# Optimization experiments

Hardware: AMD Instinct MI355X
Metric: run time of the kernel (lower is better)

Reference implementation:

```python
import jax, jax.numpy as jnp
import numpy as np

NUM_HEADS = 8
NUM_KV_HEADS = 2
PATCH = 16
STRIDE = 8
HORIZON = 96
NQ = 3
EPS_RMS = 1e-6
EPS_REVIN = 1e-5


def rms_norm(x, scale):
    return x * jax.lax.rsqrt(jnp.mean(x * x, axis=-1, keepdims=True) + EPS_RMS) * scale


def lstm_scan(xs, wi, wh, b):
    # xs: (N, T, Din); flax OptimizedLSTMCell gate order i, f, g, o
    N = xs.shape[0]
    H = wh.shape[0]

    def step(carry, x_t):
        c, h = carry
        z = x_t @ wi + h @ wh + b
        i, f, g, o = jnp.split(z, 4, axis=-1)
        c = jax.nn.sigmoid(f) * c + jax.nn.sigmoid(i) * jnp.tanh(g)
        h = jax.nn.sigmoid(o) * jnp.tanh(c)
        return (c, h), h

    init = (jnp.zeros((N, H), xs.dtype), jnp.zeros((N, H), xs.dtype))
    _, hs = jax.lax.scan(step, init, jnp.swapaxes(xs, 0, 1))
    return jnp.swapaxes(hs, 0, 1)  # (N, T, H)


def gqa(x, wq, wk, wv, wo):
    # x: (B, S, D); non-causal grouped-query attention
    B, S, D = x.shape
    hd = wq.shape[1] // NUM_HEADS
    q = (x @ wq).reshape(B, S, NUM_HEADS, hd)
    k = (x @ wk).reshape(B, S, NUM_KV_HEADS, hd)
    v = (x @ wv).reshape(B, S, NUM_KV_HEADS, hd)
    rep = NUM_HEADS // NUM_KV_HEADS
    k = jnp.repeat(k, rep, axis=2)
    v = jnp.repeat(v, rep, axis=2)
    scale = jnp.asarray(1.0 / np.sqrt(hd), x.dtype)
    attn = jax.nn.softmax(jnp.einsum('bqhd,bkhd->bhqk', q, k) * scale, axis=-1)
    out = jnp.einsum('bhqk,bkhd->bqhd', attn, v).reshape(B, S, NUM_HEADS * hd)
    return out @ wo, attn


def setup_inputs() -> dict:
    key = jax.random.key(0)
    ks = jax.random.split(key, 12)
    b, d, m, T = 8, 16, 8, 512
    H, H2 = 256, 512
    NB = 4

    def w(k, shape, fan_in):
        return jax.random.normal(k, shape, jnp.float32) / np.sqrt(fan_in)

    return {
        'series': jax.random.normal(ks[0], (b, d, m, T), jnp.float32),
        'revin_scale': jnp.ones((m,), jnp.float32),
        'revin_bias': jnp.zeros((m,), jnp.float32),
        'up_w': w(ks[1], (PATCH, H), PATCH),
        'lstm_wi': w(ks[2], (NB, H, 4 * H2), H),
        'lstm_wh': w(ks[3], (NB, H2, 4 * H2), H2),
        'lstm_b': jnp.zeros((NB, 4 * H2), jnp.float32),
        'norm_scale': jnp.ones((NB, H2), jnp.float32),
        'wq': w(ks[4], (NB, H2, H2), H2),
        'wk': w(ks[5], (NB, H2, H2 // 4), H2),
        'wv': w(ks[6], (NB, H2, H2 // 4), H2),
        'wo': w(ks[7], (NB, H2, H2), H2),
        'down_w': w(ks[8], (NB, H2, H), H2),
        'head_norm_scale': jnp.ones((H,), jnp.float32),
        'point_w': w(ks[9], (H, HORIZON), H),
        'quant_w': w(ks[10], (H, HORIZON * NQ), H),
    }


def reference(series, revin_scale, revin_bias, up_w, lstm_wi, lstm_wh, lstm_b,
              norm_scale, wq, wk, wv, wo, down_w, head_norm_scale, point_w, quant_w):
    b, d, m, T = series.shape
    num_blocks = lstm_wi.shape[0]
    H = up_w.shape[1]
    H2 = lstm_wh.shape[1]

    # RevIN instance norm over time with per-metric affine
    mean = series.mean(axis=-1, keepdims=True)
    std = jnp.sqrt(series.var(axis=-1, keepdims=True) + EPS_REVIN)
    sc = revin_scale[:, None]
    bi = revin_bias[:, None]
    normed = (series - mean) / std * sc + bi

    # Patcher (seq_len=512, patch=16, stride=8 -> 63 patches, no padding needed)
    n_p = (T - PATCH) // STRIDE + 1
    idx = jnp.arange(n_p)[:, None] * STRIDE + jnp.arange(PATCH)
    patches = normed[..., idx]            # (b, d, m, np, ps)
    x = patches @ up_w                    # (b, d, m, np, H)

    for blk in range(num_blocks):
        s = x.reshape(b * d * m, n_p, H)
        hs = lstm_scan(s, lstm_wi[blk], lstm_wh[blk], lstm_b[blk])  # (bdm, np, H2)
        # '(b d m) np h -> (b m np) d h'
        hs = hs.reshape(b, d, m, n_p, H2).transpose(0, 2, 3, 1, 4).reshape(b * m * n_p, d, H2)
        nrm = rms_norm(hs, norm_scale[blk])
        mix, _ = gqa(nrm, wq[blk], wk[blk], wv[blk], wo[blk])
        bel = mix @ down_w[blk]           # (bmnp, d, H)
        # '(b m np) d h -> b d m np h'
        x = bel.reshape(b, m, n_p, d, H).transpose(0, 3, 1, 2, 4)

    # pooling_mode == 'last' with device mixer: last block's belief at last patch
    last = x[:, :, :, -1, :]              # (b, d, m, H)
    nb = rms_norm(last, head_norm_scale)
    point = nb @ point_w                  # (b, d, m, horizon)
    quant = (nb @ quant_w).reshape(b, d, m, HORIZON, NQ).transpose(4, 0, 1, 2, 3)

    def denorm(y):
        return (y - bi) / sc * std + mean

    point_u = denorm(point)
    quant_u = denorm(quant)               # broadcasts over leading quantile axis
    return jnp.concatenate([point_u[None], quant_u], axis=0)  # (1+NQ, b, d, m, horizon)
```

## Files before the change

kernel.cpp:

```cpp
#include <hip/hip_runtime.h>
#include <hip/hip_bf16.h>

#define NP 63

typedef __attribute__((ext_vector_type(8))) short short8;
typedef __attribute__((ext_vector_type(4))) float f32x4;
typedef __attribute__((ext_vector_type(4))) int i32x4;
typedef unsigned char uchar;

__device__ __forceinline__ float sigf(float x){ return 1.0f/(1.0f+expf(-x)); }
__device__ __forceinline__ float u2f(ushort u){ __hip_bfloat16 h; *(ushort*)&h = u; return __bfloat162float(h); }
__device__ __forceinline__ ushort f2u(float f){ __hip_bfloat16 h = __float2bfloat16(f); return *(ushort*)&h; }

__global__ void __launch_bounds__(256) k_revin(const float* __restrict__ series,
    float* __restrict__ meanv, float* __restrict__ stdv, int* __restrict__ bar)
{
  int n = blockIdx.x, tid = threadIdx.x;
  if(n==0 && tid<64) bar[tid] = 0;
  __shared__ float s1[256], s2[256];
  const float* p = series + n*512;
  float a = 0.f, b = 0.f;
  for(int t=tid;t<512;t+=256){ float v=p[t]; a+=v; b+=v*v; }
  s1[tid]=a; s2[tid]=b; __syncthreads();
  for(int s=128;s>0;s>>=1){
    if(tid<s){ s1[tid]+=s1[tid+s]; s2[tid]+=s2[tid+s]; }
    __syncthreads();
  }
  if(tid==0){
    float mu = s1[0]*(1.f/512.f);
    float var = fmaxf(s2[0]*(1.f/512.f) - mu*mu, 0.f);
    meanv[n]=mu; stdv[n]=sqrtf(var+1e-5f);
  }
}

__global__ void __launch_bounds__(256) k_patch(const float* __restrict__ series,
    const float* __restrict__ rs, const float* __restrict__ rb,
    const float* __restrict__ up_w, const float* __restrict__ meanv,
    const float* __restrict__ stdv, ushort* __restrict__ x)
{
  int n = blockIdx.x, tid = threadIdx.x;
  int m = n & 7;
  __shared__ float sn[512];
  float mu = meanv[n], sd = stdv[n];
  float A = rs[m]/sd, C = rb[m] - mu*A;
  const float* p = series + n*512;
  for(int t=tid;t<512;t+=256) sn[t] = p[t]*A + C;
  __syncthreads();
  float w[16];
  #pragma unroll
  for(int i=0;i<16;i++) w[i] = up_w[i*256+tid];
  ushort* xo = x + n*(NP*256);
  for(int pi=0;pi<NP;pi++){
    float acc=0.f;
    #pragma unroll
    for(int i=0;i<16;i++) acc = fmaf(sn[pi*8+i], w[i], acc);
    xo[pi*256+tid] = f2u(acc);
  }
}

__global__ void __launch_bounds__(256) k_wod(const float* __restrict__ wo,
    const float* __restrict__ dw, float* __restrict__ wod)
{
  int i = blockIdx.x, blk = blockIdx.y, tid = threadIdx.x;
  __shared__ float row[512];
  const float* wr = wo + (blk*512 + i)*512;
  for(int k=tid;k<512;k+=256) row[k]=wr[k];
  __syncthreads();
  const float* d = dw + blk*512*256;
  float acc=0.f;
  for(int k=0;k<512;k++) acc = fmaf(row[k], d[k*256+tid], acc);
  wod[(blk*512+i)*256+tid]=acc;
}

__global__ void __launch_bounds__(256) k_tr_wodt(const float* __restrict__ wod, ushort* __restrict__ wodt)
{
  __shared__ float tile[32][33];
  int blk = blockIdx.z;
  int n0 = blockIdx.x*32, k0 = blockIdx.y*32;
  int tid = threadIdx.x;
  #pragma unroll
  for(int i=0;i<4;i++){
    int idx = tid + 256*i; int kl = idx>>5, nl = idx&31;
    tile[kl][nl] = wod[blk*512*256 + (k0+kl)*256 + n0+nl];
  }
  __syncthreads();
  #pragma unroll
  for(int i=0;i<4;i++){
    int idx = tid + 256*i; int nl = idx>>5, kl = idx&31;
    wodt[blk*256*512 + (n0+nl)*512 + k0+kl] = f2u(tile[kl][nl]);
  }
}

__global__ void __launch_bounds__(256) k_tr_lstmw(const float* __restrict__ wi,
    const float* __restrict__ wh, ushort* __restrict__ wt)
{
  __shared__ float tile[32][33];
  int blk = blockIdx.z;
  int n0 = blockIdx.x*32, k0 = blockIdx.y*32;
  int tid = threadIdx.x;
  #pragma unroll
  for(int i=0;i<4;i++){
    int idx = tid + 256*i; int kl = idx>>5, nl = idx&31;
    int k = k0+kl, n = n0+nl;
    float v = (k<256) ? wi[blk*256*2048 + k*2048 + n]
                      : wh[blk*512*2048 + (k-256)*2048 + n];
    tile[kl][nl] = v;
  }
  __syncthreads();
  #pragma unroll
  for(int i=0;i<4;i++){
    int idx = tid + 256*i; int nl = idx>>5, kl = idx&31;
    wt[blk*2048*768 + (n0+nl)*768 + k0+kl] = f2u(tile[kl][nl]);
  }
}

__global__ void __launch_bounds__(256) k_tr_qkvw(const float* __restrict__ wq,
    const float* __restrict__ wk, const float* __restrict__ wv,
    const float* __restrict__ ns, ushort* __restrict__ wqkvt)
{
  __shared__ float tile[32][33];
  int blk = blockIdx.z;
  int n0 = blockIdx.x*32, k0 = blockIdx.y*32;
  int tid = threadIdx.x;
  #pragma unroll
  for(int i=0;i<4;i++){
    int idx = tid + 256*i; int kl = idx>>5, nl = idx&31;
    int k = k0+kl, n = n0+nl;
    float v;
    if(n < 512)      v = wq[blk*512*512 + k*512 + n];
    else if(n < 640) v = wk[blk*512*128 + k*128 + (n-512)];
    else             v = wv[blk*512*128 + k*128 + (n-640)];
    tile[kl][nl] = v * ns[blk*512 + k];
  }
  __syncthreads();
  #pragma unroll
  for(int i=0;i<4;i++){
    int idx = tid + 256*i; int nl = idx>>5, kl = idx&31;
    wqkvt[blk*768*512 + (n0+nl)*512 + k0+kl] = f2u(tile[kl][nl]);
  }
}

__global__ void __launch_bounds__(256,1) k_lstm_scan(
    const ushort* __restrict__ x, ushort* __restrict__ hs,
    const ushort* __restrict__ wt, const float* __restrict__ bias,
    uchar* __restrict__ flags, int tagbase)
{
  __shared__ __align__(16) short Bwh[128*512];
  __shared__ __align__(16) ushort hstage[64*32];
  int fb = blockIdx.x;
  int g = (fb & 7) | ((fb >> 4) & 8);
  int y = (fb >> 3) & 15;
  int n0 = g*64, jj0 = y*32;
  int tid = threadIdx.x;
  int wv = tid>>6, lane = tid&63, quad = lane>>4, l16 = lane&15;
  int wrow = wv>>1, wcol = wv&1;

  for(int i=tid; i<8192; i+=256){
    int c = i>>6, kb = i&63;
    short8 v = *(const short8*)(wt + ((c>>5)*512 + jj0 + (c&31))*768 + 256 + kb*8);
    *(short8*)((char*)Bwh + c*1024 + ((kb*16) ^ ((c&7)<<4))) = v;
  }
  int jj = jj0 + wcol*16 + l16;
  short8 bwi[4][8];
  #pragma unroll
  for(int gg=0; gg<4; gg++){
    const ushort* wp = wt + (gg*512 + jj)*768 + quad*8;
    #pragma unroll
    for(int ck=0; ck<8; ck++) bwi[gg][ck] = *(const short8*)(wp + ck*32);
  }
  float bI=bias[jj], bF=bias[512+jj], bG=bias[1024+jj], bO=bias[1536+jj];
  float cs[2][4];
  #pragma unroll
  for(int a=0;a<2;a++){
    #pragma unroll
    for(int r=0;r<4;r++) cs[a][r]=0.f;
  }
  const ushort* xb0 = x  + (n0 + wrow*32 + l16)*(NP*256) + quad*8;
  const ushort* hb0 = hs + (n0 + wrow*32 + l16)*(NP*512) + quad*8;
  int xorb = (l16&7)<<4;
  uchar* myflag = flags + g*16 + y;
  const uchar* gflags = flags + g*16;
  __syncthreads();

  for(int t=0; t<NP; ++t){
    f32x4 acc[4][2];
    #pragma unroll
    for(int gg=0; gg<4; gg++){ acc[gg][0]=(f32x4){0.f,0.f,0.f,0.f}; acc[gg][1]=(f32x4){0.f,0.f,0.f,0.f}; }

    #pragma unroll
    for(int ck=0; ck<8; ck++){
      short8 a0 = *(const short8*)(xb0 + t*256 + ck*32);
      short8 a1 = *(const short8*)(xb0 + 16*(NP*256) + t*256 + ck*32);
      #pragma unroll
      for(int gg=0; gg<4; gg++){
        acc[gg][0] = __builtin_amdgcn_mfma_f32_16x16x32_bf16(a0, bwi[gg][ck], acc[gg][0], 0,0,0);
        acc[gg][1] = __builtin_amdgcn_mfma_f32_16x16x32_bf16(a1, bwi[gg][ck], acc[gg][1], 0,0,0);
      }
    }

    if(t > 0){
      if(tid==0){
        uint tag = (uint)(tagbase + t);
        while(1){
          i32x4 f;
          asm volatile("global_load_dwordx4 %0, %1, off sc0 sc1\n\ts_waitcnt vmcnt(0)"
                       : "=&v"(f) : "v"(gflags) : "memory");
          uint ok = 1u;
          #pragma unroll
          for(int q=0;q<4;q++){
            uint w = (uint)f[q];
            if(( w      &0xffu) < tag) ok=0;
            if(((w>>8 ) &0xffu) < tag) ok=0;
            if(((w>>16) &0xffu) < tag) ok=0;
            if( (w>>24)         < tag) ok=0;
          }
          if(ok) break;
          __builtin_amdgcn_s_sleep(1);
        }
      }
      __syncthreads();

      const ushort* hb = hb0 + (t-1)*512;
      #pragma unroll
      for(int ck=0; ck<16; ck++){
        short8 a0 = *(const short8*)(hb + ck*32);
        short8 a1 = *(const short8*)(hb + 16*(NP*512) + ck*32);
        #pragma unroll
        for(int gg=0; gg<4; gg++){
          int c = gg*32 + wcol*16 + l16;
          short8 bh = *(short8*)((char*)Bwh + c*1024 + ((ck*64 + quad*16) ^ xorb));
          acc[gg][0] = __builtin_amdgcn_mfma_f32_16x16x32_bf16(a0, bh, acc[gg][0], 0,0,0);
          acc[gg][1] = __builtin_amdgcn_mfma_f32_16x16x32_bf16(a1, bh, acc[gg][1], 0,0,0);
        }
      }
    }

    #pragma unroll
    for(int a=0;a<2;a++){
      #pragma unroll
      for(int r=0;r<4;r++){
        int rowl = wrow*32 + a*16 + quad*4 + r;
        float zi=acc[0][a][r]+bI, zf=acc[1][a][r]+bF, zg=acc[2][a][r]+bG, zo=acc[3][a][r]+bO;
        float c = sigf(zf)*cs[a][r] + sigf(zi)*tanhf(zg);
        cs[a][r] = c;
        float hv = sigf(zo)*tanhf(c);
        int coll = wcol*16 + l16;
        int off = rowl*64 + ((coll*2) ^ (((rowl>>2)&3)<<4));
        *(ushort*)((char*)hstage + off) = f2u(hv);
      }
    }
    __syncthreads();
    {
      int rowl = tid>>2, c0b = (tid&3)*16;
      int off = rowl*64 + (c0b ^ (((rowl>>2)&3)<<4));
      i32x4 vv = *(const i32x4*)((const char*)hstage + off);
      ushort* gp = hs + ((size_t)(n0+rowl)*NP + t)*512 + jj0 + (tid&3)*8;
      asm volatile("global_store_dwordx4 %0, %1, off sc0 sc1" :: "v"(gp), "v"(vv) : "memory");
    }
    __syncthreads();
    if(tid==0 && t < NP-1){
      uint v = (uint)(tagbase + t + 1);
      asm volatile("global_store_byte %0, %1, off sc0 sc1" :: "v"(myflag), "v"(v) : "memory");
    }
  }
}

__global__ void __launch_bounds__(256) k_qkv_m(
    const ushort* __restrict__ hs, const ushort* __restrict__ wqkvt,
    ushort* __restrict__ qkv)
{
  __shared__ short As[128*40];
  __shared__ short Bs[128*40];
  __shared__ float rvs[128];
  int tid = threadIdx.x;
  int r0 = blockIdx.x*128, c0 = blockIdx.y*128;
  int wv = tid>>6, lane = tid&63, quad = lane>>4, l16 = lane&15;
  int wrow = wv>>1, wcol = wv&1;
  int arow0 = tid>>2, akp = tid&3;
  const ushort* aptr[2];
  #pragma unroll
  for(int i=0;i<2;i++){
    int r = r0 + arow0 + i*64;
    int bq = r/8064; int rr = r - bq*8064;
    int m = rr/1008; int rem = rr - m*1008;
    int p = rem>>4; int d = rem&15;
    int n = (bq*16+d)*8+m;
    aptr[i] = hs + (n*NP+p)*512 + akp*8;
  }
  f32x4 acc[4][4];
  #pragma unroll
  for(int b=0;b<4;b++){
    #pragma unroll
    for(int a=0;a<4;a++) acc[b][a] = (f32x4){0.f,0.f,0.f,0.f};
  }
  float ssq0 = 0.f, ssq1 = 0.f;
  for(int k0=0;k0<512;k0+=32){
    {
      short8 av = *(const short8*)(aptr[0] + k0);
      *(short8*)&As[arow0*40 + akp*8] = av;
      #pragma unroll
      for(int e=0;e<8;e++){ float vv = u2f((ushort)av[e]); ssq0 = fmaf(vv, vv, ssq0); }
    }
    {
      short8 av = *(const short8*)(aptr[1] + k0);
      *(short8*)&As[(arow0+64)*40 + akp*8] = av;
      #pragma unroll
      for(int e=0;e<8;e++){ float vv = u2f((ushort)av[e]); ssq1 = fmaf(vv, vv, ssq1); }
    }
    #pragma unroll
    for(int i=0;i<2;i++){
      int pc = tid + 256*i; int rl=pc>>2, kp=pc&3;
      *(short8*)&Bs[rl*40+kp*8] = *(const short8*)(wqkvt + (c0+rl)*512 + k0 + kp*8);
    }
    __syncthreads();
    short8 af[4], bfr[4];
    #pragma unroll
    for(int a=0;a<4;a++) af[a] = *(short8*)&As[(wrow*64 + a*16 + l16)*40 + quad*8];
    #pragma unroll
    for(int b=0;b<4;b++) bfr[b] = *(short8*)&Bs[(wcol*64 + b*16 + l16)*40 + quad*8];
    #pragma unroll
    for(int b=0;b<4;b++){
      #pragma unroll
      for(int a=0;a<4;a++)
        acc[b][a] = __builtin_amdgcn_mfma_f32_16x16x32_bf16(af[a], bfr[b], acc[b][a], 0,0,0);
    }
    __syncthreads();
  }
  ssq0 += __shfl_xor(ssq0, 1); ssq0 += __shfl_xor(ssq0, 2);
  ssq1 += __shfl_xor(ssq1, 1); ssq1 += __shfl_xor(ssq1, 2);
  if(akp==0){
    rvs[arow0]    = rsqrtf(ssq0*(1.f/512.f)+1e-6f);
    rvs[arow0+64] = rsqrtf(ssq1*(1.f/512.f)+1e-6f);
  }
  __syncthreads();
  #pragma unroll
  for(int a=0;a<4;a++){
    #pragma unroll
    for(int rg=0;rg<4;rg++){
      int rowl = wrow*64 + a*16 + quad*4 + rg;
      int rw = r0 + rowl;
      float rv = rvs[rowl];
      #pragma unroll
      for(int b=0;b<4;b++){
        int c = c0 + wcol*64 + b*16 + l16;
        qkv[rw*768 + c] = f2u(acc[b][a][rg] * rv);
      }
    }
  }
}

__global__ void __launch_bounds__(256) k_attn(ushort* __restrict__ qkv)
{
  int r3 = blockIdx.x, h = blockIdx.y;
  int tid = threadIdx.x;
  __shared__ float qs[16][64];
  __shared__ float ks[16][65];
  __shared__ float vs[16][64];
  __shared__ float P[16][17];
  ushort* base = qkv + r3*16*768;
  int xx = tid&63, s4 = tid>>6;
  int kvh = (h>>2)*64;
  #pragma unroll
  for(int a=0;a<4;a++){
    int s = s4 + 4*a;
    qs[s][xx] = u2f(base[s*768 + h*64 + xx]);
    ks[s][xx] = u2f(base[s*768 + 512 + kvh + xx]);
    vs[s][xx] = u2f(base[s*768 + 640 + kvh + xx]);
  }
  __syncthreads();
  int i = tid>>4, j = tid&15;
  float sc = 0.f;
  #pragma unroll
  for(int xq=0;xq<64;xq++) sc = fmaf(qs[i][xq], ks[j][xq], sc);
  P[i][j] = sc*0.125f;
  __syncthreads();
  float row[16];
  #pragma unroll
  for(int jj=0;jj<16;jj++) row[jj] = P[i][jj];
  float mx = row[0];
  #pragma unroll
  for(int jj=1;jj<16;jj++) mx = fmaxf(mx, row[jj]);
  float sum = 0.f;
  #pragma unroll
  for(int jj=0;jj<16;jj++) sum += expf(row[jj]-mx);
  float pme = expf(row[j]-mx)/sum;
  __syncthreads();
  P[i][j] = pme;
  __syncthreads();
  #pragma unroll
  for(int a=0;a<4;a++){
    int s = s4 + 4*a;
    float o = 0.f;
    #pragma unroll
    for(int jj=0;jj<16;jj++) o = fmaf(P[s][jj], vs[jj][xx], o);
    base[s*768 + h*64 + xx] = f2u(o);
  }
}

__global__ void __launch_bounds__(256) k_bel_m(
    const ushort* __restrict__ qkv, const ushort* __restrict__ wodt,
    ushort* __restrict__ x)
{
  __shared__ short As[128*40];
  __shared__ short Bs[128*40];
  int tid = threadIdx.x;
  int r0 = blockIdx.x*128, c0 = blockIdx.y*128;
  int wv = tid>>6, lane = tid&63, quad = lane>>4, l16 = lane&15;
  int wrow = wv>>1, wcol = wv&1;
  int arow0 = tid>>2, akp = tid&3;
  const ushort* aptr0 = qkv + (r0+arow0)*768 + akp*8;
  const ushort* aptr1 = qkv + (r0+arow0+64)*768 + akp*8;
  f32x4 acc[4][4];
  #pragma unroll
  for(int b=0;b<4;b++){
    #pragma unroll
    for(int a=0;a<4;a++) acc[b][a] = (f32x4){0.f,0.f,0.f,0.f};
  }
  for(int k0=0;k0<512;k0+=32){
    *(short8*)&As[arow0*40 + akp*8]      = *(const short8*)(aptr0 + k0);
    *(short8*)&As[(arow0+64)*40 + akp*8] = *(const short8*)(aptr1 + k0);
    #pragma unroll
    for(int i=0;i<2;i++){
      int pc = tid + 256*i; int rl=pc>>2, kp=pc&3;
      *(short8*)&Bs[rl*40+kp*8] = *(const short8*)(wodt + (c0+rl)*512 + k0 + kp*8);
    }
    __syncthreads();
    short8 af[4], bfr[4];
    #pragma unroll
    for(int a=0;a<4;a++) af[a] = *(short8*)&As[(wrow*64 + a*16 + l16)*40 + quad*8];
    #pragma unroll
    for(int b=0;b<4;b++) bfr[b] = *(short8*)&Bs[(wcol*64 + b*16 + l16)*40 + quad*8];
    #pragma unroll
    for(int b=0;b<4;b++){
      #pragma unroll
      for(int a=0;a<4;a++)
        acc[b][a] = __builtin_amdgcn_mfma_f32_16x16x32_bf16(af[a], bfr[b], acc[b][a], 0,0,0);
    }
    __syncthreads();
  }
  #pragma unroll
  for(int a=0;a<4;a++){
    #pragma unroll
    for(int rg=0;rg<4;rg++){
      int rw = r0 + wrow*64 + a*16 + quad*4 + rg;
      int bq = rw/8064; int rr = rw - bq*8064;
      int m = rr/1008; int rem = rr - m*1008;
      int p = rem>>4; int d = rem&15;
      int n = (bq*16+d)*8+m;
      ushort* xo = x + (n*NP+p)*256;
      #pragma unroll
      for(int b=0;b<4;b++){
        int c = c0 + wcol*64 + b*16 + l16;
        xo[c] = f2u(acc[b][a][rg]);
      }
    }
  }
}

__global__ void __launch_bounds__(256) k_head(const ushort* __restrict__ x,
    const float* __restrict__ meanv, const float* __restrict__ stdv,
    const float* __restrict__ rs, const float* __restrict__ rb,
    const float* __restrict__ hns, const float* __restrict__ pw,
    const float* __restrict__ qw, float* __restrict__ out)
{
  int n = blockIdx.x, tid = threadIdx.x;
  __shared__ float nb[256];
  __shared__ float red[256];
  float v = u2f(x[(n*NP + 62)*256 + tid]);
  red[tid] = v*v; __syncthreads();
  for(int s=128;s>0;s>>=1){
    if(tid<s) red[tid]+=red[tid+s];
    __syncthreads();
  }
  float rinv = rsqrtf(red[0]*(1.f/256.f)+1e-6f);
  nb[tid] = v*rinv*hns[tid];
  __syncthreads();
  int m = n&7;
  float mu=meanv[n], sd=stdv[n], sc=rs[m], bi=rb[m];
  for(int col=tid; col<384; col+=256){
    float acc=0.f;
    int slot, hh;
    if(col < 96){
      for(int k=0;k<256;k++) acc = fmaf(nb[k], pw[k*96+col], acc);
      slot = 0; hh = col;
    } else {
      int cq = col-96;
      for(int k=0;k<256;k++) acc = fmaf(nb[k], qw[k*288+cq], acc);
      int qi = cq - (cq/3)*3;
      slot = 1 + qi; hh = cq/3;
    }
    float y = (acc - bi)/sc*sd + mu;
    out[(slot*1024 + n)*96 + hh] = y;
  }
}

extern "C" void kernel_launch(void* const* d_in, const int* in_sizes, int n_in,
                              void* d_out, int out_size, void* d_ws, size_t ws_size,
                              hipStream_t stream)
{
  const float* series    = (const float*)d_in[0];
  const float* rs        = (const float*)d_in[1];
  const float* rb        = (const float*)d_in[2];
  const float* up_w      = (const float*)d_in[3];
  const float* lstm_wi   = (const float*)d_in[4];
  const float* lstm_wh   = (const float*)d_in[5];
  const float* lstm_b    = (const float*)d_in[6];
  const float* norm_scale= (const float*)d_in[7];
  const float* wq        = (const float*)d_in[8];
  const float* wk        = (const float*)d_in[9];
  const float* wv        = (const float*)d_in[10];
  const float* wo        = (const float*)d_in[11];
  const float* down_w    = (const float*)d_in[12];
  const float* head_ns   = (const float*)d_in[13];
  const float* point_w   = (const float*)d_in[14];
  const float* quant_w   = (const float*)d_in[15];
  float* out = (float*)d_out;

  float* ws = (float*)d_ws;
  float*  meanv = ws;
  float*  stdv  = meanv + 1024;
  float*  rmsi  = stdv  + 1024;
  float*  cst   = rmsi  + 64512;
  float*  wodf  = cst   + 524288;
  ushort* xbuf  = (ushort*)(wodf + 524288);
  ushort* hsb   = xbuf  + 16515072;
  ushort* qkvb  = hsb   + 33030144;
  ushort* wt    = qkvb  + 49545216;
  ushort* wqkvt = wt    + 6291456;
  ushort* wodt  = wqkvt + 1572864;
  int*    bar   = (int*)cst;

  k_revin<<<1024,256,0,stream>>>(series, meanv, stdv, bar);
  k_patch<<<1024,256,0,stream>>>(series, rs, rb, up_w, meanv, stdv, xbuf);
  k_wod<<<dim3(512,4),256,0,stream>>>(wo, down_w, wodf);
  k_tr_wodt<<<dim3(8,16,4),256,0,stream>>>(wodf, wodt);
  k_tr_lstmw<<<dim3(64,24,4),256,0,stream>>>(lstm_wi, lstm_wh, wt);
  k_tr_qkvw<<<dim3(24,16,4),256,0,stream>>>(wq, wk, wv, norm_scale, wqkvt);

  for(int blk=0; blk<4; blk++){
    const ushort* wt_b = wt + blk*2048*768;
    const float*  bb   = lstm_b + blk*2048;
    k_lstm_scan<<<256,256,0,stream>>>(xbuf, hsb, wt_b, bb, (uchar*)bar, blk*NP);
    k_qkv_m<<<dim3(504,6),256,0,stream>>>(hsb, wqkvt + blk*768*512, qkvb);
    k_attn<<<dim3(4032,8),256,0,stream>>>(qkvb);
    k_bel_m<<<dim3(504,2),256,0,stream>>>(qkvb, wodt + blk*256*512, xbuf);
  }
  k_head<<<1024,256,0,stream>>>(xbuf, meanv, stdv, rs, rb, head_ns, point_w, quant_w, out);
}
```

Measured before the change: 3.631 ms.

## Detect same-XCD groups in LSTM scan and use cheaper cache scopes

Each LSTM scan block records its XCD id at startup, and the blocks of a 16-block group check whether they all landed on the same XCD. If they did, the per-step hidden-state stores and flag stores/polls drop from system scope (sc0 sc1) to device or L2-local scope. The goal is to cut the latency of the inter-block step handshake. In exchange it adds a startup rendezvous and extra barrier memory. Correctness depends on L2 coherence within an XCD, and on the later kernels seeing non-sc stores after the kernel boundary.

```diff
diff --git a/kernel.cpp b/kernel.cpp
--- a/kernel.cpp
+++ b/kernel.cpp
@@ -16,7 +16,7 @@
     float* __restrict__ meanv, float* __restrict__ stdv, int* __restrict__ bar)
 {
   int n = blockIdx.x, tid = threadIdx.x;
-  if(n==0 && tid<64) bar[tid] = 0;
+  if(n==0){ for(int i=tid;i<320;i+=256) bar[i]=0; }
   __shared__ float s1[256], s2[256];
   const float* p = series + n*512;
   float a = 0.f, b = 0.f;
@@ -143,10 +143,11 @@
 __global__ void __launch_bounds__(256,1) k_lstm_scan(
     const ushort* __restrict__ x, ushort* __restrict__ hs,
     const ushort* __restrict__ wt, const float* __restrict__ bias,
-    uchar* __restrict__ flags, int tagbase)
+    uchar* __restrict__ flags, int tagbase, uchar* __restrict__ detect)
 {
   __shared__ __align__(16) short Bwh[128*512];
   __shared__ __align__(16) ushort hstage[64*32];
+  __shared__ int fastflag;
   int fb = blockIdx.x;
   int g = (fb & 7) | ((fb >> 4) & 8);
   int y = (fb >> 3) & 15;
@@ -180,7 +181,34 @@
   int xorb = (l16&7)<<4;
   uchar* myflag = flags + g*16 + y;
   const uchar* gflags = flags + g*16;
-  __syncthreads();
+
+  if(tid==0){
+    uint xcc = __builtin_amdgcn_s_getreg(63508) & 0xfu;
+    uint myid = xcc + 1u;
+    uchar* dp = detect + g*16 + y;
+    asm volatile("global_store_byte %0, %1, off sc0 sc1" :: "v"(dp), "v"(myid) : "memory");
+    const uchar* dq = detect + g*16;
+    while(1){
+      i32x4 f;
+      asm volatile("global_load_dwordx4 %0, %1, off sc0 sc1\n\ts_waitcnt vmcnt(0)"
+                   : "=&v"(f) : "v"(dq) : "memory");
+      uint allnz=1u, alleq=1u;
+      #pragma unroll
+      for(int q=0;q<4;q++){
+        uint w=(uint)f[q];
+        #pragma unroll
+        for(int b=0;b<4;b++){
+          uint bv = (w>>(8*b))&0xffu;
+          if(bv==0u) allnz=0u;
+          else if(bv!=myid) alleq=0u;
+        }
+      }
+      if(allnz){ fastflag = (int)alleq; break; }
+      __builtin_amdgcn_s_sleep(2);
+    }
+  }
+  __syncthreads();
+  const int FAST = fastflag;
 
   for(int t=0; t<NP; ++t){
     f32x4 acc[4][2];
@@ -203,8 +231,12 @@
         uint tag = (uint)(tagbase + t);
         while(1){
           i32x4 f;
-          asm volatile("global_load_dwordx4 %0, %1, off sc0 sc1\n\ts_waitcnt vmcnt(0)"
-                       : "=&v"(f) : "v"(gflags) : "memory");
+          if(FAST)
+            asm volatile("global_load_dwordx4 %0, %1, off sc0\n\ts_waitcnt vmcnt(0)"
+                         : "=&v"(f) : "v"(gflags) : "memory");
+          else
+            asm volatile("global_load_dwordx4 %0, %1, off sc0 sc1\n\ts_waitcnt vmcnt(0)"
+                         : "=&v"(f) : "v"(gflags) : "memory");
           uint ok = 1u;
           #pragma unroll
           for(int q=0;q<4;q++){
@@ -255,12 +287,18 @@
       int off = rowl*64 + (c0b ^ (((rowl>>2)&3)<<4));
       i32x4 vv = *(const i32x4*)((const char*)hstage + off);
       ushort* gp = hs + ((size_t)(n0+rowl)*NP + t)*512 + jj0 + (tid&3)*8;
-      asm volatile("global_store_dwordx4 %0, %1, off sc0 sc1" :: "v"(gp), "v"(vv) : "memory");
+      if(FAST)
+        asm volatile("global_store_dwordx4 %0, %1, off" :: "v"(gp), "v"(vv) : "memory");
+      else
+        asm volatile("global_store_dwordx4 %0, %1, off sc0 sc1" :: "v"(gp), "v"(vv) : "memory");
     }
     __syncthreads();
     if(tid==0 && t < NP-1){
       uint v = (uint)(tagbase + t + 1);
-      asm volatile("global_store_byte %0, %1, off sc0 sc1" :: "v"(myflag), "v"(v) : "memory");
+      if(FAST)
+        asm volatile("global_store_byte %0, %1, off" :: "v"(myflag), "v"(v) : "memory");
+      else
+        asm volatile("global_store_byte %0, %1, off sc0 sc1" :: "v"(myflag), "v"(v) : "memory");
     }
   }
 }
@@ -540,7 +578,8 @@
   for(int blk=0; blk<4; blk++){
     const ushort* wt_b = wt + blk*2048*768;
     const float*  bb   = lstm_b + blk*2048;
-    k_lstm_scan<<<256,256,0,stream>>>(xbuf, hsb, wt_b, bb, (uchar*)bar, blk*NP);
+    k_lstm_scan<<<256,256,0,stream>>>(xbuf, hsb, wt_b, bb, (uchar*)bar, blk*NP,
+                                      (uchar*)bar + 256 + blk*256);
     k_qkv_m<<<dim3(504,6),256,0,stream>>>(hsb, wqkvt + blk*768*512, qkvb);
     k_attn<<<dim3(4032,8),256,0,stream>>>(qkvb);
     k_bel_m<<<dim3(504,2),256,0,stream>>>(qkvb, wodt + blk*256*512, xbuf);
```

Result: no change. 3.605 ms (-0.7%).
